# Kernel optimization log

Hardware: AMD Instinct MI355X
Metric: run time of the kernel (lower is better)

Reference implementation:

```python
import math
import jax, jax.numpy as jnp
import numpy as np

CHUNK = 64  # chunk_size


def sinusoidal_pe(L, H):
    # PositionalEncoding2: standard sinusoidal table added to input (eval mode, no dropout)
    pos = jnp.arange(L, dtype=jnp.float32)[:, None]
    div = jnp.exp(jnp.arange(0, H, 2, dtype=jnp.float32) * (-math.log(10000.0) / H))
    pe = jnp.zeros((L, H), dtype=jnp.float32)
    pe = pe.at[:, 0::2].set(jnp.sin(pos * div))
    pe = pe.at[:, 1::2].set(jnp.cos(pos * div))
    return pe


def setup_inputs() -> dict:
    key = jax.random.key(0)
    ks = jax.random.split(key, 8)
    B, T, D, H, Dv = 8, 4096, 512, 512, 512
    s = 0.02
    return {
        "data": jax.random.normal(ks[0], (B, T, D), dtype=jnp.float32),
        "v0": jax.random.normal(ks[1], (B, Dv), dtype=jnp.float32),
        "v1": jax.random.normal(ks[2], (B, Dv), dtype=jnp.float32),
        "W_embed": jax.random.normal(ks[3], (D, H), dtype=jnp.float32) * s,
        "b_embed": jnp.zeros((H,), dtype=jnp.float32),
        "Wx": jax.random.normal(ks[4], (H, 2), dtype=jnp.float32) * s,
        "Wv": jax.random.normal(ks[5], (Dv, 2), dtype=jnp.float32) * s,
        "b_f": jnp.zeros((2,), dtype=jnp.float32),
    }


def reference(data, v0, v1, W_embed, b_embed, Wx, Wv, b_f):
    B, T, D = data.shape
    H = W_embed.shape[1]
    n_chunks = T // CHUNK  # chunks per batch row

    # add_pos: Linear embed + positional encoding, scaled by sqrt(chunk_size)
    h = data @ W_embed + b_embed                       # [B, T, H]
    h = (h + sinusoidal_pe(T, H)[None]) * math.sqrt(CHUNK)

    x = h.reshape(B * n_chunks, CHUNK, H)              # chunked view

    key = jax.random.key(42)
    F = None
    for i, v in enumerate((v0, v1)):
        v_rep = jnp.repeat(v, n_chunks, axis=0)        # [B*n_chunks, Dv]
        # filter model: per-token 2-way logits conditioned on chunk value vector
        logits = x @ Wx + (v_rep @ Wv)[:, None, :] + b_f  # [B*n_chunks, CHUNK, 2]
        # StochasticMultinomialTensor.sample(): gumbel-max one-hot, straight-through
        g = jax.random.gumbel(jax.random.fold_in(key, i), logits.shape, dtype=logits.dtype)
        hard = jax.nn.one_hot(jnp.argmax(logits + g, axis=-1), 2, dtype=logits.dtype)
        soft = jax.nn.softmax(logits, axis=-1)
        samp = soft + jax.lax.stop_gradient(hard - soft)
        f = samp[:, :, 0].reshape(B, T)                # de_chunk -> [B, T]
        F = f if F is None else F * f

    mask = F > 0.5                                     # [B, T]
    vals = h * F[..., None]                            # data[F>0.5] * F scaling

    # ragged compaction: stable-sort selected tokens to the front of each row
    order = jnp.argsort((~mask).astype(jnp.int32), axis=1)   # stable
    packed = jnp.take_along_axis(vals, order[:, :, None], axis=1)  # [B, T, H]
    lens = mask.sum(-1)                                # per-row selected count
    keep = jnp.arange(T)[None, :] < lens[:, None]
    # pad_sequence equivalent, padded to T (superset of max(lens)); zeros beyond lens
    return packed * keep[..., None]
```

## Files before the change

### kernel.cpp

```cpp
#include <hip/hip_runtime.h>
#include <stdint.h>


#define NB 8
#define NT 4096
#define ND 512
#define NH 512
#define NTOK (NB * NT)

typedef __attribute__((ext_vector_type(8))) short short8;
typedef __attribute__((ext_vector_type(4))) float f32x4;

#define WS_WEX   0
#define WS_PEX   8192
#define WS_VWV   73728
#define WS_LENS  76048
#define WS_WT    76096
#define WS_MASK  731456
#define WS_ABF16 1310720

__device__ inline void threefry2x32(uint32_t k0, uint32_t k1, uint32_t x0, uint32_t x1,
                                    uint32_t& y0, uint32_t& y1) {
  uint32_t ks2 = k0 ^ k1 ^ 0x1BD11BDAu;
  x0 += k0; x1 += k1;
#define TFR(r) { x0 += x1; x1 = (x1 << (r)) | (x1 >> (32 - (r))); x1 ^= x0; }
  TFR(13) TFR(15) TFR(26) TFR(6)   x0 += k1;  x1 += ks2 + 1u;
  TFR(17) TFR(29) TFR(16) TFR(24)  x0 += ks2; x1 += k0 + 2u;
  TFR(13) TFR(15) TFR(26) TFR(6)   x0 += k0;  x1 += k1 + 3u;
  TFR(17) TFR(29) TFR(16) TFR(24)  x0 += k1;  x1 += ks2 + 4u;
  TFR(13) TFR(15) TFR(26) TFR(6)   x0 += ks2; x1 += k0 + 5u;
#undef TFR
  y0 = x0; y1 = x1;
}

__device__ inline uint32_t rb_bits(uint32_t k0, uint32_t k1, uint32_t idx) {
  uint32_t y0, y1;
  threefry2x32(k0, k1, 0u, idx, y0, y1);
  return y0 ^ y1;
}

__device__ inline double gumbel_from_bits(uint32_t bits) {
  uint32_t m = bits >> 9;
  float u = m ? (float)m * 1.1920928955078125e-07f : 1.17549435082228751e-38f;
  double lu = log((double)u);
  return -log(-lu);
}

__device__ inline uint16_t f2bf(float f) {
  union { float f; uint32_t u; } v; v.f = f;
  uint32_t u = v.u;
  return (uint16_t)((u + 0x7FFFu + ((u >> 16) & 1u)) >> 16);
}

__device__ inline double wredd(double v) {
#pragma unroll
  for (int o = 32; o > 0; o >>= 1) v += __shfl_xor(v, o, 64);
  return v;
}

__device__ inline void fsincos(double x, double& sv, double& cv) {
  const double invpio2 = 6.36619772367581382433e-01;
  const double pio2_1  = 1.57079632673412561417e+00;
  const double pio2_1t = 6.07710050650619224932e-11;
  double fn = floor(x * invpio2 + 0.5);
  int n = (int)fn;
  double r = x - fn * pio2_1;
  r = r - fn * pio2_1t;
  double z = r * r;
  const double S1 = -1.66666666666666324348e-01, S2 = 8.33333333332248946124e-03,
               S3 = -1.98412698298579493134e-04, S4 = 2.75573137070700676789e-06,
               S5 = -2.50507602534068634195e-08, S6 = 1.58969099521155010221e-10;
  const double C1 = 4.16666666666666019037e-02, C2 = -1.38888888888741095749e-03,
               C3 = 2.48015872894767294178e-05, C4 = -2.75573143513906633035e-07,
               C5 = 2.08757232129817482790e-09, C6 = -1.13596475577881948265e-11;
  double ss = r + r * z * (S1 + z * (S2 + z * (S3 + z * (S4 + z * (S5 + z * S6)))));
  double cc = 1.0 + z * (-0.5 + z * (C1 + z * (C2 + z * (C3 + z * (C4 + z * (C5 + z * C6))))));
  int q = n & 3;
  sv = (q == 0) ? ss : (q == 1) ? cc : (q == 2) ? -ss : -cc;
  cv = (q == 0) ? cc : (q == 1) ? -ss : (q == 2) ? -cc : ss;
}

__device__ inline void gld_lds16(const void* g, void* l) {
  __builtin_amdgcn_global_load_lds(
      (const __attribute__((address_space(1))) void*)g,
      (__attribute__((address_space(3))) void*)l, 16, 0, 0);
}

__global__ __launch_bounds__(64) void k_prep(
    const float* __restrict__ v0, const float* __restrict__ v1,
    const float* __restrict__ W, const float* __restrict__ be,
    const float* __restrict__ Wx, const float* __restrict__ Wv,
    char* __restrict__ ws) {
  double* Wex = (double*)(ws + WS_WEX);
  double* pex = (double*)(ws + WS_PEX);
  double* vWv = (double*)(ws + WS_VWV);
  uint16_t* Wt = (uint16_t*)(ws + WS_WT);
  __shared__ double divs[256];
  int blk = blockIdx.x;
  int lane = threadIdx.x;

  if (blk < 512) {
    int d = blk;
    double a0 = 0.0, a1 = 0.0;
    for (int it = 0; it < 8; ++it) {
      int h = it * 64 + lane;
      double w = (double)W[d * 512 + h];
      a0 += w * (double)Wx[2 * h];
      a1 += w * (double)Wx[2 * h + 1];
    }
    a0 = wredd(a0); a1 = wredd(a1);
    if (lane == 0) { Wex[2 * d] = a0; Wex[2 * d + 1] = a1; }
  } else if (blk < 4608) {
    const double c2 = -2.0 * 9.210340371976184 / 512.0;
    for (int it = 0; it < 4; ++it) {
      int f = it * 64 + lane;
      divs[f] = exp((double)f * c2);
    }
    __syncthreads();
    int t = blk - 512;
    double td = (double)t;
    double a0 = 0.0, a1 = 0.0;
    for (int it = 0; it < 8; ++it) {
      int h = it * 64 + lane;
      double dv = divs[h >> 1];
      double sv, cv;
      fsincos(td * dv, sv, cv);
      double pe = (h & 1) ? cv : sv;
      double pb = pe + (double)be[h];
      a0 += pb * (double)Wx[2 * h];
      a1 += pb * (double)Wx[2 * h + 1];
    }
    a0 = wredd(a0); a1 = wredd(a1);
    if (lane == 0) { pex[2 * t] = a0; pex[2 * t + 1] = a1; }
  } else if (blk < 4624) {
    int q = blk - 4608;
    int i = q >> 3, b = q & 7;
    const float* v = i ? v1 : v0;
    double a0 = 0.0, a1 = 0.0;
    for (int it = 0; it < 8; ++it) {
      int d = it * 64 + lane;
      double x = (double)v[b * 512 + d];
      a0 += x * (double)Wv[2 * d];
      a1 += x * (double)Wv[2 * d + 1];
    }
    a0 = wredd(a0); a1 = wredd(a1);
    if (lane == 0) { vWv[(i * 8 + b) * 2] = a0; vWv[(i * 8 + b) * 2 + 1] = a1; }
  } else {
    int kk = blk - 4624;
    for (int it = 0; it < 8; ++it) {
      int n = it * 64 + lane;
      Wt[(size_t)n * 512 + kk] = f2bf(W[kk * 512 + n]);
    }
  }
}

__global__ __launch_bounds__(256) void k_dot(
    const float* __restrict__ data, const float* __restrict__ bfp,
    const char* __restrict__ wsc, int* __restrict__ mask,
    uint16_t* __restrict__ Abf) {
  const double* Wex = (const double*)(wsc + WS_WEX);
  const double* pex = (const double*)(wsc + WS_PEX);
  const double* vWv = (const double*)(wsc + WS_VWV);

  int wid = threadIdx.x >> 6;
  int lane = threadIdx.x & 63;
  int kbase = (blockIdx.x * 4 + wid) * 4;

  double w0[8], w1[8];
#pragma unroll
  for (int u = 0; u < 8; ++u) {
    double2 wv = *(const double2*)(Wex + 2 * (u * 64 + lane));
    w0[u] = wv.x; w1[u] = wv.y;
  }

  float x[4][8];
  double d0s[4], d1s[4];
#pragma unroll
  for (int tt = 0; tt < 4; ++tt) {
    int k = kbase + tt;
    const float* dpt = data + (size_t)k * 512 + lane;
#pragma unroll
    for (int u = 0; u < 8; ++u) x[tt][u] = dpt[u * 64];

    double d0 = 0.0, d1 = 0.0;
#pragma unroll
    for (int u = 0; u < 8; ++u) {
      double xd = (double)x[tt][u];
      d0 += xd * w0[u];
      d1 += xd * w1[u];
    }
    d0s[tt] = wredd(d0);
    d1s[tt] = wredd(d1);
  }

  int dec = 0;
  if (lane < 16) {
    int tt = lane >> 2, i = (lane >> 1) & 1, j = lane & 1;
    double da = (tt & 2) ? ((tt & 1) ? d0s[3] : d0s[2])
                         : ((tt & 1) ? d0s[1] : d0s[0]);
    double db = (tt & 2) ? ((tt & 1) ? d1s[3] : d1s[2])
                         : ((tt & 1) ? d1s[1] : d1s[0]);
    double dj = j ? db : da;
    int kk = kbase + tt;
    int bb = kk >> 12, ttok = kk & 4095;
    uint32_t key0, key1;
    threefry2x32(0u, 42u, 0u, (uint32_t)i, key0, key1);
    double lj = 8.0 * (dj + pex[ttok * 2 + j]) + (double)bfp[j];
    double z = lj + vWv[(i * 8 + bb) * 2 + j]
                 + gumbel_from_bits(rb_bits(key0, key1, (uint32_t)(2 * kk + j)));
    double zo = __shfl_xor(z, 1, 64);
    dec = (z >= zo) ? 1 : 0;
  }
  unsigned long long bal = __ballot(dec);
  if (lane < 4)
    mask[kbase + lane] =
        (int)((bal >> (lane * 4)) & (bal >> (lane * 4 + 2)) & 1ULL);

#pragma unroll
  for (int tt = 0; tt < 4; ++tt) {
    int keep = (int)((bal >> (tt * 4)) & (bal >> (tt * 4 + 2)) & 1ULL);
    if (keep) {
      uint16_t* ap = Abf + (size_t)(kbase + tt) * 512 + lane;
#pragma unroll
      for (int u = 0; u < 8; ++u) ap[u * 64] = f2bf(x[tt][u]);
    }
  }
}

__global__ __launch_bounds__(1024) void k_scan(
    int* __restrict__ morder, int* __restrict__ lens) {
  __shared__ int wsum[16];
  int b = blockIdx.x, tid = threadIdx.x;
  int wid = tid >> 6, lane = tid & 63;
  int t0 = tid * 4;
  int4 mv = *(const int4*)(morder + b * 4096 + t0);
  int m[4] = {mv.x, mv.y, mv.z, mv.w};
  int p = m[0] + m[1] + m[2] + m[3];

  int s = p;
#pragma unroll
  for (int off = 1; off < 64; off <<= 1) {
    int v = __shfl_up(s, off, 64);
    if (lane >= off) s += v;
  }
  if (lane == 63) wsum[wid] = s;
  __syncthreads();
  if (wid == 0) {
    int w = (lane < 16) ? wsum[lane] : 0;
#pragma unroll
    for (int off = 1; off < 16; off <<= 1) {
      int v = __shfl_up(w, off, 64);
      if (lane >= off) w += v;
    }
    if (lane < 16) wsum[lane] = w;
  }
  __syncthreads();
  int run = ((wid > 0) ? wsum[wid - 1] : 0) + s - p;
  int base = b * 4096;
  if (m[0]) morder[base + run] = t0 + 0;
  run += m[0];
  if (m[1]) morder[base + run] = t0 + 1;
  run += m[1];
  if (m[2]) morder[base + run] = t0 + 2;
  run += m[2];
  if (m[3]) morder[base + run] = t0 + 3;
  if (tid == 1023) lens[b] = wsum[15];
}

__global__ __launch_bounds__(256) void k_zero(
    const char* __restrict__ wsc, float* __restrict__ out) {
  const int* lens = (const int*)(wsc + WS_LENS);
  int b = blockIdx.y;
  int j = blockIdx.x * 4 + (threadIdx.x >> 6);
  if (j < lens[b]) return;
  int lane = threadIdx.x & 63;
  float4 z = {0.f, 0.f, 0.f, 0.f};
  float* op = out + ((size_t)(b * 4096 + j)) * 512 + lane * 8;
  *(float4*)op = z;
  *(float4*)(op + 4) = z;
}

#define BM 64
#define BN 128
#define BK 32

__global__ __launch_bounds__(256) void k_gemm(
    const uint16_t* __restrict__ Abf, const float* __restrict__ be,
    const char* __restrict__ wsc, float* __restrict__ out) {
  const uint16_t* Wt = (const uint16_t*)(wsc + WS_WT);
  const int* order = (const int*)(wsc + WS_MASK);
  const int* lens = (const int*)(wsc + WS_LENS);

  int cum[9];
  cum[0] = 0;
#pragma unroll
  for (int i = 0; i < 8; ++i) cum[i + 1] = cum[i] + lens[i];
  int S = cum[8];

  int bid = blockIdx.x;
  int nb = bid & 3;
  int G = (bid >> 2) * BM;
  if (G >= S) return;

  int tid = threadIdx.x;
  int wave = tid >> 6, lane = tid & 63;
  int wm = wave & 1, wn = wave >> 1;
  int quad = lane >> 4, l15 = lane & 15;
  int srow = lane >> 2;
  int scol = (lane & 3) * 8;

  __shared__ __align__(16) uint16_t As[BM * BK];
  __shared__ __align__(16) uint16_t Bs[BN * BK];

  f32x4 acc[2][4] = {};

  int lr = wave * 16 + srow;
  int pg0 = G + lr;
  int b0 = 0, pin0 = pg0;
#pragma unroll
  for (int i = 1; i < 8; ++i)
    if (pg0 >= cum[i]) { b0 = i; pin0 = pg0 - cum[i]; }
  if (pg0 >= S) { b0 = 0; pin0 = 0; }
  int t0r = order[(b0 << 12) + pin0];
  const uint16_t* a0p = Abf + (((size_t)(b0 << 12) + t0r) << 9) + scol;
  const uint16_t* gB = Wt + (size_t)(nb * BN) * 512;
  const uint16_t* b0p = gB + (size_t)lr * 512 + scol;
  const uint16_t* b1p = b0p + (size_t)64 * 512;

  uint16_t* lA = As + (size_t)(wave * 16) * BK;
  uint16_t* lB = Bs + (size_t)(wave * 16) * BK;

  for (int k0 = 0; k0 < 512; k0 += BK) {
    gld_lds16(a0p + k0, lA);
    gld_lds16(b0p + k0, lB);
    gld_lds16(b1p + k0, lB + 64 * BK);
    __syncthreads();

    short8 af[2], bfr[4];
#pragma unroll
    for (int mi = 0; mi < 2; ++mi)
      af[mi] = *(const short8*)&As[(wm * 32 + mi * 16 + l15) * BK + quad * 8];
#pragma unroll
    for (int ni = 0; ni < 4; ++ni)
      bfr[ni] = *(const short8*)&Bs[(wn * 64 + ni * 16 + l15) * BK + quad * 8];
#pragma unroll
    for (int mi = 0; mi < 2; ++mi)
#pragma unroll
      for (int ni = 0; ni < 4; ++ni)
        acc[mi][ni] = __builtin_amdgcn_mfma_f32_16x16x32_bf16(af[mi], bfr[ni], acc[mi][ni], 0, 0, 0);
    __syncthreads();
  }

  int* ords = (int*)As;
  int* orows = (int*)Bs;
  if (tid < 64) {
    int pg = G + tid;
    int bb = 0, pp = pg;
#pragma unroll
    for (int i = 1; i < 8; ++i)
      if (pg >= cum[i]) { bb = i; pp = pg - cum[i]; }
    bool val = pg < S;
    ords[tid] = val ? order[(bb << 12) + pp] : 0;
    orows[tid] = val ? ((bb << 12) + pp) : -1;
  }
  __syncthreads();

  const float c1 = -0.01798894603951557739f;
#pragma unroll
  for (int ni = 0; ni < 4; ++ni) {
    int n = nb * BN + wn * 64 + ni * 16 + l15;
    float dv = __expf((float)(n & ~1) * c1);
    float ben = be[n];
#pragma unroll
    for (int mi = 0; mi < 2; ++mi) {
#pragma unroll
      for (int r = 0; r < 4; ++r) {
        int lrow = wm * 32 + mi * 16 + quad * 4 + r;
        int oj = orows[lrow];
        if (oj >= 0) {
          int t = ords[lrow];
          float ph = (float)t * dv;
          float pe = (n & 1) ? __cosf(ph) : __sinf(ph);
          out[((size_t)oj) * 512 + n] = 8.0f * (acc[mi][ni][r] + ben + pe);
        }
      }
    }
  }
}

extern "C" void kernel_launch(void* const* d_in, const int* in_sizes, int n_in,
                              void* d_out, int out_size, void* d_ws, size_t ws_size,
                              hipStream_t stream) {
  const float* data = (const float*)d_in[0];
  const float* v0   = (const float*)d_in[1];
  const float* v1   = (const float*)d_in[2];
  const float* W    = (const float*)d_in[3];
  const float* be   = (const float*)d_in[4];
  const float* Wx   = (const float*)d_in[5];
  const float* Wv   = (const float*)d_in[6];
  const float* bfp  = (const float*)d_in[7];
  char* ws = (char*)d_ws;
  float* out = (float*)d_out;
  uint16_t* Abf = (uint16_t*)(ws + WS_ABF16);

  hipLaunchKernelGGL(k_prep, dim3(5136), dim3(64), 0, stream, v0, v1, W, be, Wx, Wv, ws);
  hipLaunchKernelGGL(k_dot, dim3(2048), dim3(256), 0, stream,
                     data, bfp, (const char*)ws, (int*)(ws + WS_MASK), Abf);
  hipLaunchKernelGGL(k_scan, dim3(8), dim3(1024), 0, stream,
                     (int*)(ws + WS_MASK), (int*)(ws + WS_LENS));
  hipLaunchKernelGGL(k_zero, dim3(1024, 8), dim3(256), 0, stream, (const char*)ws, out);
  hipLaunchKernelGGL(k_gemm, dim3(2048), dim3(256), 0, stream,
                     Abf, be, (const char*)ws, out);
}
```

Measured before the change: 164.9 us.

## Fold zero-fill into idle GEMM blocks and vectorize k_dot loads and stores

The separate k_zero launch is removed. GEMM grid blocks beyond those needed for the S selected rows now zero-fill the padded output rows of each batch row, using a grid-stride loop over the total count of unselected rows. This saves one kernel launch and lets the zero-fill writes overlap with the GEMM tiles. k_dot also switches to float4 data loads and 4-wide bf16 stores by permuting which hidden indices each lane owns, with the embedding-weight loads permuted to match. The trade-off is that zeroing work is now bounded by the idle GEMM blocks, and the reduction order changes slightly.

```diff
diff --git a/kernel.cpp b/kernel.cpp
--- a/kernel.cpp
+++ b/kernel.cpp
@@ -9,6 +9,7 @@
 #define NTOK (NB * NT)
 
 typedef __attribute__((ext_vector_type(8))) short short8;
+typedef __attribute__((ext_vector_type(4))) short short4v;
 typedef __attribute__((ext_vector_type(4))) float f32x4;
 
 #define WS_WEX   0
@@ -168,9 +169,10 @@
 
   double w0[8], w1[8];
 #pragma unroll
-  for (int u = 0; u < 8; ++u) {
-    double2 wv = *(const double2*)(Wex + 2 * (u * 64 + lane));
-    w0[u] = wv.x; w1[u] = wv.y;
+  for (int e = 0; e < 8; ++e) {
+    int h = (e >> 2) * 256 + lane * 4 + (e & 3);
+    double2 wv = *(const double2*)(Wex + 2 * h);
+    w0[e] = wv.x; w1[e] = wv.y;
   }
 
   float x[4][8];
@@ -178,16 +180,18 @@
 #pragma unroll
   for (int tt = 0; tt < 4; ++tt) {
     int k = kbase + tt;
-    const float* dpt = data + (size_t)k * 512 + lane;
-#pragma unroll
-    for (int u = 0; u < 8; ++u) x[tt][u] = dpt[u * 64];
+    const float4* dpt = (const float4*)(data + (size_t)k * 512 + lane * 4);
+    float4 xa = dpt[0];
+    float4 xb = dpt[64];
+    x[tt][0] = xa.x; x[tt][1] = xa.y; x[tt][2] = xa.z; x[tt][3] = xa.w;
+    x[tt][4] = xb.x; x[tt][5] = xb.y; x[tt][6] = xb.z; x[tt][7] = xb.w;
 
     double d0 = 0.0, d1 = 0.0;
 #pragma unroll
-    for (int u = 0; u < 8; ++u) {
-      double xd = (double)x[tt][u];
-      d0 += xd * w0[u];
-      d1 += xd * w1[u];
+    for (int e = 0; e < 8; ++e) {
+      double xd = (double)x[tt][e];
+      d0 += xd * w0[e];
+      d1 += xd * w1[e];
     }
     d0s[tt] = wredd(d0);
     d1s[tt] = wredd(d1);
@@ -220,9 +224,15 @@
   for (int tt = 0; tt < 4; ++tt) {
     int keep = (int)((bal >> (tt * 4)) & (bal >> (tt * 4 + 2)) & 1ULL);
     if (keep) {
-      uint16_t* ap = Abf + (size_t)(kbase + tt) * 512 + lane;
-#pragma unroll
-      for (int u = 0; u < 8; ++u) ap[u * 64] = f2bf(x[tt][u]);
+      uint16_t* ap = Abf + (size_t)(kbase + tt) * 512 + lane * 4;
+      short4v s0, s1;
+#pragma unroll
+      for (int q = 0; q < 4; ++q) {
+        s0[q] = (short)f2bf(x[tt][q]);
+        s1[q] = (short)f2bf(x[tt][4 + q]);
+      }
+      *(short4v*)ap = s0;
+      *(short4v*)(ap + 256) = s1;
     }
   }
 }
@@ -267,19 +277,6 @@
   if (tid == 1023) lens[b] = wsum[15];
 }
 
-__global__ __launch_bounds__(256) void k_zero(
-    const char* __restrict__ wsc, float* __restrict__ out) {
-  const int* lens = (const int*)(wsc + WS_LENS);
-  int b = blockIdx.y;
-  int j = blockIdx.x * 4 + (threadIdx.x >> 6);
-  if (j < lens[b]) return;
-  int lane = threadIdx.x & 63;
-  float4 z = {0.f, 0.f, 0.f, 0.f};
-  float* op = out + ((size_t)(b * 4096 + j)) * 512 + lane * 8;
-  *(float4*)op = z;
-  *(float4*)(op + 4) = z;
-}
-
 #define BM 64
 #define BN 128
 #define BK 32
@@ -298,11 +295,35 @@
   int S = cum[8];
 
   int bid = blockIdx.x;
+  int tid = threadIdx.x;
+  int nWB = (S + BM - 1) / BM;
+
+  if (bid >= nWB * 4) {
+    int vid = bid - nWB * 4;
+    int V = (int)gridDim.x - nWB * 4;
+    int zcum[9];
+    zcum[0] = 0;
+#pragma unroll
+    for (int i = 0; i < 8; ++i) zcum[i + 1] = zcum[i] + (4096 - lens[i]);
+    int Z = zcum[8];
+    int wv = tid >> 6, lane = tid & 63;
+    float4 zz = {0.f, 0.f, 0.f, 0.f};
+    for (int z = vid * 4 + wv; z < Z; z += V * 4) {
+      int bb = 0, off = z;
+#pragma unroll
+      for (int i = 1; i < 8; ++i)
+        if (z >= zcum[i]) { bb = i; off = z - zcum[i]; }
+      int j = lens[bb] + off;
+      float* op = out + ((size_t)(bb * 4096 + j)) * 512 + lane * 8;
+      *(float4*)op = zz;
+      *(float4*)(op + 4) = zz;
+    }
+    return;
+  }
+
   int nb = bid & 3;
   int G = (bid >> 2) * BM;
-  if (G >= S) return;
-
-  int tid = threadIdx.x;
+
   int wave = tid >> 6, lane = tid & 63;
   int wm = wave & 1, wn = wave >> 1;
   int quad = lane >> 4, l15 = lane & 15;
@@ -408,7 +429,6 @@
                      data, bfp, (const char*)ws, (int*)(ws + WS_MASK), Abf);
   hipLaunchKernelGGL(k_scan, dim3(8), dim3(1024), 0, stream,
                      (int*)(ws + WS_MASK), (int*)(ws + WS_LENS));
-  hipLaunchKernelGGL(k_zero, dim3(1024, 8), dim3(256), 0, stream, (const char*)ws, out);
   hipLaunchKernelGGL(k_gemm, dim3(2048), dim3(256), 0, stream,
                      Abf, be, (const char*)ws, out);
 }
```

New measurement: 158.5 us, median of 2. 1.04x faster.
